# Optimization experiments

Measured on AMD Instinct MI355X. Metric: run time of the kernel, lower is better.

Reference implementation:

```python
import jax, jax.numpy as jnp
import numpy as np

H = 16      # num heads
DH = 64     # head dim
D = H * DH  # hidden = 1024

def setup_inputs() -> dict:
    key = jax.random.key(0)
    ks = jax.random.split(key, 8)
    B, S = 4, 2048
    scale = 1.0 / np.sqrt(D)
    return {
        "hidden_states": jax.random.normal(ks[0], (B, S, D), dtype=jnp.float32),
        "attention_mask": jnp.zeros((B, S, S), dtype=jnp.float32),
        "Wq": jax.random.normal(ks[1], (D, D), dtype=jnp.float32) * scale,
        "bq": jnp.zeros((D,), dtype=jnp.float32),
        "Wk": jax.random.normal(ks[2], (D, D), dtype=jnp.float32) * scale,
        "bk": jnp.zeros((D,), dtype=jnp.float32),
        "Wv": jax.random.normal(ks[3], (D, D), dtype=jnp.float32) * scale,
        "bv": jnp.zeros((D,), dtype=jnp.float32),
    }

def _split_heads(x):
    B, S, _ = x.shape
    return x.reshape(B, S, H, DH).transpose(0, 2, 1, 3)  # [B,H,S,dh]

def reference(hidden_states, attention_mask, Wq, bq, Wk, bk, Wv, bv):
    q = _split_heads(hidden_states @ Wq + bq)
    k = _split_heads(hidden_states @ Wk + bk)
    v = _split_heads(hidden_states @ Wv + bv)
    scores = jnp.einsum("bhqd,bhkd->bhqk", q, k) / jnp.sqrt(jnp.float32(DH))
    scores = scores + attention_mask[:, None, :, :]
    probs = jax.nn.softmax(scores, axis=-1)  # dropout p=0 (eval) -> identity
    ctx = jnp.einsum("bhqk,bhkd->bhqd", probs, v)
    B, _, S, _ = ctx.shape
    return ctx.transpose(0, 2, 1, 3).reshape(B, S, H * DH)
```

## Files before the change

kernel.cpp:

```cpp
#include <hip/hip_runtime.h>

typedef __bf16 bf16;
typedef __bf16 bf16x8 __attribute__((ext_vector_type(8)));
typedef __bf16 bf16x4 __attribute__((ext_vector_type(4)));
typedef float floatx4 __attribute__((ext_vector_type(4)));
typedef unsigned int uint4t __attribute__((ext_vector_type(4)));

typedef __attribute__((address_space(1))) void gvoid;
typedef __attribute__((address_space(3))) void lvoid;
#define ASYNC_COPY16(gp, lp) \
  __builtin_amdgcn_global_load_lds((gvoid*)(gp), (lvoid*)(lp), 16, 0, 0)

#define NB 4
#define SQ 2048
#define DMODEL 1024
#define NH 16
#define HD 64
#define MTOK (NB * SQ)
#define LOG2E 1.44269504088896f

#define XB_OFF 0ull
#define WT_OFF (16ull * 1024 * 1024)
#define Q_OFF  (22ull * 1024 * 1024)
#define K_OFF  (38ull * 1024 * 1024)
#define V_OFF  (54ull * 1024 * 1024)
#define FLG_OFF (70ull * 1024 * 1024)

__global__ __launch_bounds__(256) void prep(
    const float* __restrict__ x, bf16* __restrict__ xb,
    const float* __restrict__ w0, const float* __restrict__ w1,
    const float* __restrict__ w2, bf16* __restrict__ wt,
    const float* __restrict__ mask, int* __restrict__ flags) {
  __shared__ float tlds[32][33];
  int blk = blockIdx.x;
  int t = threadIdx.x;
  if (blk < 1024) {
    size_t base = (size_t)blk * 2048 + t;
    const float4* xin = (const float4*)x;
    bf16x4* xo = (bf16x4*)xb;
#pragma unroll
    for (int j = 0; j < 8; j++) {
      float4 v = xin[base + j * 256];
      bf16x4 o;
      o[0] = (bf16)v.x; o[1] = (bf16)v.y; o[2] = (bf16)v.z; o[3] = (bf16)v.w;
      xo[base + j * 256] = o;
    }
  } else if (blk < 4096) {
    int tidx = blk - 1024;
    int z = tidx >> 10;
    int rem = tidx & 1023;
    int kb = ((rem >> 5) & 31) * 32, nb = (rem & 31) * 32;
    const float* w = (z == 0) ? w0 : (z == 1) ? w1 : w2;
    bf16* out = wt + (size_t)z * DMODEL * DMODEL;
    int tx = t & 31, ty = t >> 5;
#pragma unroll
    for (int i = 0; i < 4; i++)
      tlds[ty + 8 * i][tx] = w[(size_t)(kb + ty + 8 * i) * DMODEL + nb + tx];
    __syncthreads();
#pragma unroll
    for (int i = 0; i < 4; i++)
      out[(size_t)(nb + ty + 8 * i) * DMODEL + kb + tx] = (bf16)tlds[tx][ty + 8 * i];
  } else {
    int midx = blk - 4096;
    int kt = midx & 31, qt = (midx >> 5) & 15, b = midx >> 9;
    const float* mb = mask + ((size_t)b * SQ + qt * 128) * SQ + kt * 64;
    int row = t >> 1, half = t & 1;
    const float4* p = (const float4*)(mb + (size_t)row * SQ + half * 32);
    bool nz = false;
#pragma unroll
    for (int i = 0; i < 8; i++) {
      float4 vv = p[i];
      nz |= (vv.x != 0.f) | (vv.y != 0.f) | (vv.z != 0.f) | (vv.w != 0.f);
    }
    int* acc = (int*)tlds;
    if (t == 0) acc[0] = 0;
    __syncthreads();
    unsigned long long m = __ballot(nz);
    if ((t & 63) == 0 && m) atomicOr(acc, 1);
    __syncthreads();
    if (t == 0) flags[(b * 16 + qt) * 32 + kt] = acc[0];
  }
}

#define BK 64
__global__ __launch_bounds__(256) void qkv(
    const bf16* __restrict__ xb,
    const bf16* __restrict__ wt,
    const float* __restrict__ biasq, const float* __restrict__ biask,
    const float* __restrict__ biasv,
    bf16* __restrict__ q, bf16* __restrict__ k, bf16* __restrict__ v) {
  __shared__ bf16 As[128 * BK];
  __shared__ bf16 Bs[128 * BK];

  int id = blockIdx.x;
  int local = id >> 3;
  int mt = ((id & 7) << 3) | (local & 7);
  int nt = local >> 3;
  int t = threadIdx.x;

  int mat = nt >> 3;
  int nbase = (nt & 7) * 128;
  const bf16* wmat = wt + (size_t)mat * DMODEL * DMODEL;
  const float* bias = (mat == 0) ? biasq : (mat == 1) ? biask : biasv;
  bf16* outp = (mat == 0) ? q : (mat == 1) ? k : v;

  int lane = t & 63, wid = t >> 6;
  int quad = lane >> 4, l16 = lane & 15;
  int wm = (wid & 1) * 64, wn = (wid >> 1) * 64;
  int xq = quad ^ (l16 & 7);

  floatx4 acc[4][4] = {};

  for (int kb = 0; kb < DMODEL; kb += BK) {
    __syncthreads();
#pragma unroll
    for (int p = 0; p < 4; p++) {
      int i2 = p * 256 + t;
      int row = i2 >> 3;
      int gch = (i2 ^ row) & 7;
      ASYNC_COPY16(xb + (size_t)(mt * 128 + row) * DMODEL + kb + gch * 8,
                   As + i2 * 8);
      ASYNC_COPY16(wmat + (size_t)(nbase + row) * DMODEL + kb + gch * 8,
                   Bs + i2 * 8);
    }
    __syncthreads();

#pragma unroll
    for (int kc = 0; kc < BK; kc += 32) {
      int xc = (kc >> 3) ^ xq;
      bf16x8 af[4], bfr[4];
#pragma unroll
      for (int mi = 0; mi < 4; mi++)
        af[mi] = *(const bf16x8*)(As + (wm + mi * 16 + l16) * BK + xc * 8);
#pragma unroll
      for (int ni = 0; ni < 4; ni++)
        bfr[ni] = *(const bf16x8*)(Bs + (wn + ni * 16 + l16) * BK + xc * 8);
      if (mat < 2) {
#pragma unroll
        for (int mi = 0; mi < 4; mi++)
#pragma unroll
          for (int ni = 0; ni < 4; ni++)
            acc[mi][ni] = __builtin_amdgcn_mfma_f32_16x16x32_bf16(
                bfr[ni], af[mi], acc[mi][ni], 0, 0, 0);
      } else {
#pragma unroll
        for (int mi = 0; mi < 4; mi++)
#pragma unroll
          for (int ni = 0; ni < 4; ni++)
            acc[mi][ni] = __builtin_amdgcn_mfma_f32_16x16x32_bf16(
                af[mi], bfr[ni], acc[mi][ni], 0, 0, 0);
      }
    }
  }

  int mg0 = mt * 128 + wm;
  if (mat < 2) {
    float qscale = (mat == 0) ? 0.125f * LOG2E : 1.0f;
#pragma unroll
    for (int ni = 0; ni < 4; ni++) {
      int n0 = nbase + wn + ni * 16 + quad * 4;
      int h = n0 >> 6, d0 = n0 & 63;
      float4 bv4 = *(const float4*)(bias + n0);
#pragma unroll
      for (int mi = 0; mi < 4; mi++) {
        int m = mg0 + mi * 16 + l16;
        int b = m >> 11, s = m & 2047;
        bf16x4 pk;
        pk[0] = (bf16)((acc[mi][ni][0] + bv4.x) * qscale);
        pk[1] = (bf16)((acc[mi][ni][1] + bv4.y) * qscale);
        pk[2] = (bf16)((acc[mi][ni][2] + bv4.z) * qscale);
        pk[3] = (bf16)((acc[mi][ni][3] + bv4.w) * qscale);
        *(bf16x4*)(outp + (((size_t)(b * NH + h) * SQ + s) << 6) + d0) = pk;
      }
    }
  } else {
#pragma unroll
    for (int ni = 0; ni < 4; ni++) {
      int n = nbase + wn + ni * 16 + l16;
      int h = n >> 6, d = n & 63;
      float bv_ = bias[n];
#pragma unroll
      for (int mi = 0; mi < 4; mi++) {
        int m0 = mg0 + mi * 16 + quad * 4;
        int b = m0 >> 11, s = m0 & 2047;
        bf16x4 pk;
#pragma unroll
        for (int r = 0; r < 4; r++) pk[r] = (bf16)(acc[mi][ni][r] + bv_);
        *(bf16x4*)(outp + (((size_t)(b * NH + h) * HD + d) << 11) + s) = pk;
      }
    }
  }
}

__global__ __launch_bounds__(256, 4) void attn(
    const bf16* __restrict__ Q,
    const bf16* __restrict__ K,
    const bf16* __restrict__ Vt,
    const float* __restrict__ mask,
    const int* __restrict__ flags,
    float* __restrict__ out) {
  __shared__ bf16 Ks[64 * 64];
  __shared__ bf16 Vs[64 * 64];

  int bh = blockIdx.x;
  int qt = blockIdx.y;
  int b = bh >> 4, h = bh & 15;
  int t = threadIdx.x, lane = t & 63, wid = t >> 6;
  int quad = lane >> 4, l16 = lane & 15;
  int q0 = qt * 128 + wid * 32;

  const bf16* Qp = Q + ((size_t)bh * SQ + q0) * HD;
  const bf16* Kp = K + (size_t)bh * SQ * HD;
  const bf16* Vp = Vt + (size_t)bh * HD * SQ;
  const float* mp = mask + ((size_t)b * SQ + q0) * SQ;
  const int* flg = flags + (b * 16 + qt) * 32;

  bf16x8 qa[2][2];
#pragma unroll
  for (int m = 0; m < 2; m++) {
    const bf16* qr = Qp + (size_t)(m * 16 + l16) * HD;
    qa[m][0] = *(const bf16x8*)(qr + quad * 8);
    qa[m][1] = *(const bf16x8*)(qr + 32 + quad * 8);
  }

  floatx4 o[2][4] = {};
  float li[2] = {0.f, 0.f};
  int xq = quad ^ (l16 & 7);

  for (int kb = 0, kti = 0; kb < SQ; kb += 64, kti++) {
    __syncthreads();
#pragma unroll
    for (int p = 0; p < 2; p++) {
      int idx = p * 256 + t;
      int row = idx >> 3;
      int gch = (idx ^ row) & 7;
      ASYNC_COPY16(Kp + (size_t)(kb + row) * HD + gch * 8, Ks + idx * 8);
      ASYNC_COPY16(Vp + (size_t)row * SQ + kb + gch * 8, Vs + idx * 8);
    }
    __syncthreads();
    int flag = flg[kti];

    float xs[2][4][4];
    __builtin_amdgcn_s_setprio(1);
#pragma unroll
    for (int kt = 0; kt < 4; kt++) {
      const bf16* kr = Ks + (kt * 16 + l16) * 64;
      bf16x8 k0 = *(const bf16x8*)(kr + xq * 8);
      bf16x8 k1 = *(const bf16x8*)(kr + (xq ^ 4) * 8);
      floatx4 z0 = {}, z1 = {};
      z0 = __builtin_amdgcn_mfma_f32_16x16x32_bf16(k0, qa[0][0], z0, 0, 0, 0);
      z0 = __builtin_amdgcn_mfma_f32_16x16x32_bf16(k1, qa[0][1], z0, 0, 0, 0);
      z1 = __builtin_amdgcn_mfma_f32_16x16x32_bf16(k0, qa[1][0], z1, 0, 0, 0);
      z1 = __builtin_amdgcn_mfma_f32_16x16x32_bf16(k1, qa[1][1], z1, 0, 0, 0);
#pragma unroll
      for (int r = 0; r < 4; r++) { xs[0][kt][r] = z0[r]; xs[1][kt][r] = z1[r]; }
    }
    __builtin_amdgcn_s_setprio(0);
    if (flag) {
#pragma unroll
      for (int m = 0; m < 2; m++)
#pragma unroll
        for (int kt = 0; kt < 4; kt++)
#pragma unroll
          for (int r = 0; r < 4; r++)
            xs[m][kt][r] = __builtin_fmaf(
                mp[(size_t)(m * 16 + l16) * SQ + kb + kt * 16 + quad * 4 + r],
                LOG2E, xs[m][kt][r]);
    }

    bf16x8 pb[2][2];
#pragma unroll
    for (int m = 0; m < 2; m++) {
      float sum = 0.f;
      unsigned int u[4][2];
#pragma unroll
      for (int kt = 0; kt < 4; kt++) {
        float e0 = __builtin_amdgcn_exp2f(xs[m][kt][0]);
        float e1 = __builtin_amdgcn_exp2f(xs[m][kt][1]);
        float e2 = __builtin_amdgcn_exp2f(xs[m][kt][2]);
        float e3 = __builtin_amdgcn_exp2f(xs[m][kt][3]);
        sum += (e0 + e1) + (e2 + e3);
        asm("v_cvt_pk_bf16_f32 %0, %1, %2" : "=v"(u[kt][0]) : "v"(e0), "v"(e1));
        asm("v_cvt_pk_bf16_f32 %0, %1, %2" : "=v"(u[kt][1]) : "v"(e2), "v"(e3));
      }
      li[m] += sum;
#pragma unroll
      for (int f = 0; f < 2; f++) {
        unsigned int a0 = u[2 * f][0], b0 = u[2 * f + 1][0];
        unsigned int a1 = u[2 * f][1], b1 = u[2 * f + 1][1];
        asm("v_permlane32_swap_b32 %0, %1" : "+v"(a0), "+v"(b0));
        asm("v_permlane32_swap_b32 %0, %1" : "+v"(a1), "+v"(b1));
        asm("v_permlane16_swap_b32 %0, %1" : "+v"(a0), "+v"(b0));
        asm("v_permlane16_swap_b32 %0, %1" : "+v"(a1), "+v"(b1));
        uint4t w;
        w[0] = a0; w[1] = a1; w[2] = b0; w[3] = b1;
        pb[m][f] = __builtin_bit_cast(bf16x8, w);
      }
    }

    __builtin_amdgcn_s_setprio(1);
#pragma unroll
    for (int dt = 0; dt < 4; dt++) {
      const bf16* vr = Vs + (dt * 16 + l16) * 64;
      bf16x8 v0 = *(const bf16x8*)(vr + xq * 8);
      bf16x8 v1 = *(const bf16x8*)(vr + (xq ^ 4) * 8);
      o[0][dt] = __builtin_amdgcn_mfma_f32_16x16x32_bf16(v0, pb[0][0], o[0][dt], 0, 0, 0);
      o[0][dt] = __builtin_amdgcn_mfma_f32_16x16x32_bf16(v1, pb[0][1], o[0][dt], 0, 0, 0);
      o[1][dt] = __builtin_amdgcn_mfma_f32_16x16x32_bf16(v0, pb[1][0], o[1][dt], 0, 0, 0);
      o[1][dt] = __builtin_amdgcn_mfma_f32_16x16x32_bf16(v1, pb[1][1], o[1][dt], 0, 0, 0);
    }
    __builtin_amdgcn_s_setprio(0);
  }
#pragma unroll
  for (int m = 0; m < 2; m++) {
    li[m] += __shfl_xor(li[m], 16, 64);
    li[m] += __shfl_xor(li[m], 32, 64);
  }
#pragma unroll
  for (int m = 0; m < 2; m++) {
    float inv = 1.0f / li[m];
    float* op = out + ((size_t)b * SQ + q0 + m * 16 + l16) * DMODEL + h * HD;
#pragma unroll
    for (int dt = 0; dt < 4; dt++)
#pragma unroll
      for (int r = 0; r < 4; r++)
        op[dt * 16 + quad * 4 + r] = o[m][dt][r] * inv;
  }
}

extern "C" void kernel_launch(void* const* d_in, const int* in_sizes, int n_in,
                              void* d_out, int out_size, void* d_ws, size_t ws_size,
                              hipStream_t stream) {
  (void)in_sizes; (void)n_in; (void)out_size; (void)ws_size;
  const float* hs   = (const float*)d_in[0];
  const float* mask = (const float*)d_in[1];
  const float* Wq   = (const float*)d_in[2];
  const float* bq   = (const float*)d_in[3];
  const float* Wk   = (const float*)d_in[4];
  const float* bk   = (const float*)d_in[5];
  const float* Wv   = (const float*)d_in[6];
  const float* bv   = (const float*)d_in[7];
  float* out = (float*)d_out;
  char* ws = (char*)d_ws;
  bf16* xb = (bf16*)(ws + XB_OFF);
  bf16* wt = (bf16*)(ws + WT_OFF);
  bf16* q  = (bf16*)(ws + Q_OFF);
  bf16* k  = (bf16*)(ws + K_OFF);
  bf16* v  = (bf16*)(ws + V_OFF);
  int* flg = (int*)(ws + FLG_OFF);

  prep<<<1024 + 3072 + 2048, 256, 0, stream>>>(hs, xb, Wq, Wk, Wv, wt, mask, flg);
  qkv<<<1536, 256, 0, stream>>>(xb, wt, bq, bk, bv, q, k, v);
  attn<<<dim3(64, 16), 256, 0, stream>>>(q, k, v, mask, flg, out);
}
```

Baseline: 289.0 us.

## Double-buffer K/V tiles in attention to prefetch the next block during compute

```diff
diff --git a/kernel.cpp b/kernel.cpp
--- a/kernel.cpp
+++ b/kernel.cpp
@@ -199,8 +199,8 @@
     const float* __restrict__ mask,
     const int* __restrict__ flags,
     float* __restrict__ out) {
-  __shared__ bf16 Ks[64 * 64];
-  __shared__ bf16 Vs[64 * 64];
+  __shared__ bf16 Ks[2][64 * 64];
+  __shared__ bf16 Vs[2][64 * 64];
 
   int bh = blockIdx.x;
   int qt = blockIdx.y;
@@ -227,24 +227,40 @@
   float li[2] = {0.f, 0.f};
   int xq = quad ^ (l16 & 7);
 
-  for (int kb = 0, kti = 0; kb < SQ; kb += 64, kti++) {
-    __syncthreads();
-#pragma unroll
-    for (int p = 0; p < 2; p++) {
-      int idx = p * 256 + t;
-      int row = idx >> 3;
-      int gch = (idx ^ row) & 7;
-      ASYNC_COPY16(Kp + (size_t)(kb + row) * HD + gch * 8, Ks + idx * 8);
-      ASYNC_COPY16(Vp + (size_t)row * SQ + kb + gch * 8, Vs + idx * 8);
-    }
-    __syncthreads();
+  {
+    int idx0 = t, idx1 = 256 + t;
+    int r0 = idx0 >> 3, g0 = (idx0 ^ r0) & 7;
+    int r1 = idx1 >> 3, g1 = (idx1 ^ r1) & 7;
+    ASYNC_COPY16(Kp + (size_t)r0 * HD + g0 * 8, Ks[0] + idx0 * 8);
+    ASYNC_COPY16(Vp + (size_t)r0 * SQ + g0 * 8, Vs[0] + idx0 * 8);
+    ASYNC_COPY16(Kp + (size_t)r1 * HD + g1 * 8, Ks[0] + idx1 * 8);
+    ASYNC_COPY16(Vp + (size_t)r1 * SQ + g1 * 8, Vs[0] + idx1 * 8);
+  }
+
+  int cur = 0;
+  for (int kb = 0, kti = 0; kb < SQ; kb += 64, kti++, cur ^= 1) {
+    __syncthreads();
+    if (kb + 64 < SQ) {
+#pragma unroll
+      for (int p = 0; p < 2; p++) {
+        int idx = p * 256 + t;
+        int row = idx >> 3;
+        int gch = (idx ^ row) & 7;
+        ASYNC_COPY16(Kp + (size_t)(kb + 64 + row) * HD + gch * 8,
+                     Ks[cur ^ 1] + idx * 8);
+        ASYNC_COPY16(Vp + (size_t)row * SQ + kb + 64 + gch * 8,
+                     Vs[cur ^ 1] + idx * 8);
+      }
+    }
     int flag = flg[kti];
+    const bf16* Kc = Ks[cur];
+    const bf16* Vc = Vs[cur];
 
     float xs[2][4][4];
     __builtin_amdgcn_s_setprio(1);
 #pragma unroll
     for (int kt = 0; kt < 4; kt++) {
-      const bf16* kr = Ks + (kt * 16 + l16) * 64;
+      const bf16* kr = Kc + (kt * 16 + l16) * 64;
       bf16x8 k0 = *(const bf16x8*)(kr + xq * 8);
       bf16x8 k1 = *(const bf16x8*)(kr + (xq ^ 4) * 8);
       floatx4 z0 = {}, z1 = {};
@@ -301,7 +317,7 @@
     __builtin_amdgcn_s_setprio(1);
 #pragma unroll
     for (int dt = 0; dt < 4; dt++) {
-      const bf16* vr = Vs + (dt * 16 + l16) * 64;
+      const bf16* vr = Vc + (dt * 16 + l16) * 64;
       bf16x8 v0 = *(const bf16x8*)(vr + xq * 8);
       bf16x8 v1 = *(const bf16x8*)(vr + (xq ^ 4) * 8);
       o[0][dt] = __builtin_amdgcn_mfma_f32_16x16x32_bf16(v0, pb[0][0], o[0][dt], 0, 0, 0);
```

After: 297.9 us. 1.03x slower.
